# Performance work log

Hardware: AMD Instinct MI355X
Metric: run time of the kernel (lower is better)

## Reference

```python
import jax, jax.numpy as jnp
import numpy as np

D = 1024      # mapped_dim
M = 5         # num_ref_modes
H = 112
W = 112


def setup_inputs() -> dict:
    key = jax.random.key(0)
    ks = jax.random.split(key, 9)
    roi_signal = jax.random.randint(ks[0], (1, 1, H, W), 0, M, dtype=jnp.int32)
    roi_features = jax.random.normal(ks[1], (1, D, H, W), dtype=jnp.float32)
    roi_mask = jax.random.uniform(ks[2], (1, 1, H, W), dtype=jnp.float32)
    s = np.float32(1.0 / np.sqrt(D))
    patch_embed = jax.random.normal(ks[3], (M, D), dtype=jnp.float32) * np.float32(np.sqrt(2.0 / (M + D)))
    Wq = jax.random.normal(ks[4], (D, D), dtype=jnp.float32) * s
    Wk = jax.random.normal(ks[5], (D, D), dtype=jnp.float32) * s
    Wv = jax.random.normal(ks[6], (D, D), dtype=jnp.float32) * s
    bq = jnp.zeros((D,), jnp.float32)
    bk = jnp.zeros((D,), jnp.float32)
    bv = jnp.zeros((D,), jnp.float32)
    conv_w = jax.random.normal(ks[7], (1, D), dtype=jnp.float32) * s  # 1x1 conv, out=1
    conv_b = jnp.zeros((1,), jnp.float32)
    return dict(roi_signal=roi_signal, roi_features=roi_features, roi_mask=roi_mask,
                patch_embed=patch_embed, Wq=Wq, bq=bq, Wk=Wk, bk=bk, Wv=Wv, bv=bv,
                conv_w=conv_w, conv_b=conv_b)


def reference(roi_signal, roi_features, roi_mask, patch_embed, Wq, bq, Wk, bk, Wv, bv, conv_w, conv_b):
    _, _, ROI_H, ROI_W = roi_mask.shape
    d = roi_features.shape[1]
    # ref_embed: one_hot(ref_label) @ patch_embed == gather; (1,1,H,W) -> (1,H,W,D) -> (1,D,H,W)
    pe = jnp.transpose(patch_embed[roi_signal[:, 0]], (0, 3, 1, 2))
    xA = roi_features + pe
    # flatten to tokens: (D, N).T -> (N, D)
    A = xA.reshape(d, -1).T
    O = roi_features.reshape(d, -1).T
    Q = A @ Wq.T + bq
    K = O @ Wk.T + bk
    V = O @ Wv.T + bv
    scores = (Q @ K.T) / jnp.sqrt(jnp.float32(d))        # (N, N) -- dominant intermediate
    attn = jax.nn.softmax(scores, axis=-1)
    out = attn @ V                                        # (N, D)
    # 1x1 conv classification head == per-token dot with conv_w
    seg = (out @ conv_w.T + conv_b).reshape(1, 1, ROI_H, ROI_W)
    return jax.nn.sigmoid(seg.astype(jnp.float32))
```

## Files before the change

### kernel.cpp

```cpp
#include <hip/hip_runtime.h>
#include <math.h>


#define DD 1024
#define NN 12544
#define NSPLIT 5
#define NPART  10
#define NTILES 49

typedef __attribute__((ext_vector_type(8))) short short8;
typedef __attribute__((ext_vector_type(4))) float f32x4;
typedef __attribute__((ext_vector_type(4))) unsigned short ushort4_t;
typedef unsigned short ushort_t;
typedef unsigned int uint32;

__device__ __forceinline__ ushort_t f2bf(float f) {
    union { float f; uint32 u; } v; v.f = f;
    uint32 u = v.u + 0x7FFF + ((v.u >> 16) & 1);
    return (ushort_t)(u >> 16);
}

__device__ __forceinline__ void gload_lds16(const void* g, void* l) {
    __builtin_amdgcn_global_load_lds((const __attribute__((address_space(1))) uint32*)g,
                                     (__attribute__((address_space(3))) uint32*)l, 16, 0, 0);
}

__global__ void k_u(const float* __restrict__ Wv, const float* __restrict__ cw,
                    const float* __restrict__ bv, float* __restrict__ u,
                    float* __restrict__ cptr) {
    const int t = threadIdx.x;
    const int k = blockIdx.x * 256 + t;
    const int d0 = blockIdx.y * 64;
    float acc = 0.f;
#pragma unroll 16
    for (int i = 0; i < 64; ++i) acc += Wv[(size_t)(d0 + i) * DD + k] * cw[d0 + i];
    atomicAdd(&u[k], acc);
    if (blockIdx.x == 0 && t < 64) {
        float ca = bv[d0 + t] * cw[d0 + t];
        for (int off = 32; off > 0; off >>= 1) ca += __shfl_down(ca, off);
        if (t == 0) atomicAdd(cptr, ca);
    }
}

__global__ __launch_bounds__(256)
void k_prep(const float* __restrict__ rf, const int* __restrict__ sig,
            const float* __restrict__ pe, const float* __restrict__ u,
            ushort_t* __restrict__ xo, ushort_t* __restrict__ xa,
            float* __restrict__ vsc) {
    __shared__ ushort_t so[64][136];
    __shared__ ushort_t sa[64][136];
    __shared__ float pel[5 * 128];
    __shared__ float ul[128];
    __shared__ int sigl[64];
    __shared__ f32x4 red[16][16];
    const int t = threadIdx.x;
    const int n0 = blockIdx.x * 64;
    if (t < 64) sigl[t] = sig[n0 + t];
    __syncthreads();
    const int dl = t >> 4, tg = t & 15;
    const int sg[4] = {sigl[tg * 4], sigl[tg * 4 + 1], sigl[tg * 4 + 2], sigl[tg * 4 + 3]};
    const int tok = t >> 2, part = t & 3;
    f32x4 vacc = (f32x4)(0.f);

    for (int c = 0; c < 8; ++c) {
        const int d0 = c * 128;
        for (int i = t; i < 640; i += 256) pel[i] = pe[(i >> 7) * DD + d0 + (i & 127)];
        if (t < 128) ul[t] = u[d0 + t];
        __syncthreads();
#pragma unroll
        for (int s = 0; s < 8; ++s) {
            const int dli = s * 16 + dl;
            const f32x4 x = *(const f32x4*)&rf[(size_t)(d0 + dli) * NN + n0 + tg * 4];
            vacc += x * ul[dli];
            ushort_t oo[4], aa[4];
#pragma unroll
            for (int j = 0; j < 4; ++j) {
                oo[j] = f2bf(x[j]);
                aa[j] = f2bf(x[j] + pel[sg[j] * 128 + dli]);
            }
#pragma unroll
            for (int j = 0; j < 4; ++j) {
                so[tg * 4 + j][dli] = oo[j];
                sa[tg * 4 + j][dli] = aa[j];
            }
        }
        __syncthreads();
#pragma unroll
        for (int i = 0; i < 4; ++i) {
            const int off = part * 32 + i * 8;
            *(short8*)&xo[(size_t)(n0 + tok) * DD + d0 + off] = *(const short8*)&so[tok][off];
            *(short8*)&xa[(size_t)(n0 + tok) * DD + d0 + off] = *(const short8*)&sa[tok][off];
        }
        __syncthreads();
    }
    red[dl][tg] = vacc;
    __syncthreads();
    if (t < 64) {
        float s = 0.f;
#pragma unroll
        for (int i = 0; i < 16; ++i) s += ((const float*)&red[i][t >> 2])[t & 3];
        vsc[n0 + t] = s;
    }
}

__global__ void k_wcast(const float* __restrict__ Wq, const float* __restrict__ Wk,
                        ushort_t* __restrict__ wqb, ushort_t* __restrict__ wkb) {
    const int idx = (blockIdx.x * 256 + threadIdx.x) * 8;
    const float* src = blockIdx.y ? Wk : Wq;
    ushort_t* dst = blockIdx.y ? wkb : wqb;
    f32x4 a = *(const f32x4*)&src[idx];
    f32x4 b = *(const f32x4*)&src[idx + 4];
    short8 o;
#pragma unroll
    for (int j = 0; j < 4; ++j) { o[j] = (short)f2bf(a[j]); o[4 + j] = (short)f2bf(b[j]); }
    *(short8*)&dst[idx] = o;
}

__global__ __launch_bounds__(256, 2)
void k_pgemm(const ushort_t* __restrict__ xb, const ushort_t* __restrict__ wb,
             const float* __restrict__ bias, float scale, ushort_t* __restrict__ outb) {
    __shared__ ushort_t as_[128 * 64];
    __shared__ ushort_t bs_[128 * 64];
    const int t = threadIdx.x;
    const int wv = t >> 6, ln = t & 63;
    const int wr = wv >> 1, wc = wv & 1;
    const int l15 = ln & 15, lhi = ln >> 4;
    const int n0 = blockIdx.x * 128;
    const int m0 = blockIdx.y * 128;
    const int srow = wv * 32;
    const int lr = ln >> 3, lc = ln & 7;
    const int swz = lc ^ lr;

    f32x4 acc[4][4];
#pragma unroll
    for (int a = 0; a < 4; ++a)
#pragma unroll
        for (int b = 0; b < 4; ++b) acc[a][b] = (f32x4)(0.f);

    for (int kk = 0; kk < DD; kk += 64) {
        __syncthreads();
#pragma unroll
        for (int i = 0; i < 4; ++i) {
            const int tok = srow + i * 8 + lr;
            gload_lds16(wb + (size_t)(m0 + tok) * DD + kk + (swz << 3), as_ + (srow + i * 8) * 64);
            gload_lds16(xb + (size_t)(n0 + tok) * DD + kk + (swz << 3), bs_ + (srow + i * 8) * 64);
        }
        __syncthreads();
#pragma unroll
        for (int kp = 0; kp < 2; ++kp) {
            short8 af[4], bf_[4];
#pragma unroll
            for (int mi = 0; mi < 4; ++mi) {
                int r = wr * 64 + mi * 16 + l15;
                int cch = (kp * 4 + lhi) ^ (r & 7);
                af[mi] = *(const short8*)(as_ + r * 64 + cch * 8);
            }
#pragma unroll
            for (int ni = 0; ni < 4; ++ni) {
                int r = wc * 64 + ni * 16 + l15;
                int cch = (kp * 4 + lhi) ^ (r & 7);
                bf_[ni] = *(const short8*)(bs_ + r * 64 + cch * 8);
            }
#pragma unroll
            for (int mi = 0; mi < 4; ++mi)
#pragma unroll
                for (int ni = 0; ni < 4; ++ni)
                    acc[mi][ni] = __builtin_amdgcn_mfma_f32_16x16x32_bf16(
                        af[mi], bf_[ni], acc[mi][ni], 0, 0, 0);
        }
    }
    float bb[4][4];
#pragma unroll
    for (int mi = 0; mi < 4; ++mi) {
        f32x4 b4 = *(const f32x4*)&bias[m0 + wr * 64 + mi * 16 + lhi * 4];
#pragma unroll
        for (int r = 0; r < 4; ++r) bb[mi][r] = b4[r];
    }
#pragma unroll
    for (int mi = 0; mi < 4; ++mi)
#pragma unroll
        for (int ni = 0; ni < 4; ++ni) {
            ushort4_t o;
#pragma unroll
            for (int r = 0; r < 4; ++r) o[r] = f2bf((acc[mi][ni][r] + bb[mi][r]) * scale);
            *(ushort4_t*)&outb[(size_t)(n0 + wc * 64 + ni * 16 + l15) * DD +
                               m0 + wr * 64 + mi * 16 + lhi * 4] = o;
        }
}

__global__ __launch_bounds__(256, 2)
void k_attn(const ushort_t* __restrict__ qb, const ushort_t* __restrict__ kb,
            const float* __restrict__ vsc, float* __restrict__ pl,
            float* __restrict__ pa) {
    __shared__ ushort_t As[3][128 * 32];
    __shared__ ushort_t Bs[3][256 * 32];
    const int t = threadIdx.x;
    const int wv = t >> 6, ln = t & 63;
    const int wm = wv >> 1, wn = wv & 1;
    const int l15 = ln & 15, lhi = ln >> 4;

    const int g = blockIdx.x;
    const int xcd = g & 7, gq = g >> 3;
    const int L = (xcd < 2) ? xcd * 62 + gq : 124 + (xcd - 2) * 61 + gq;
    const int bx = L / NSPLIT, split = L % NSPLIT;
    const int m0 = bx * 128;

    const int srr = ln >> 2;
    const int slc = ln & 3;

    float rl[4][4], ra[4][4];
#pragma unroll
    for (int a = 0; a < 4; ++a)
#pragma unroll
        for (int b = 0; b < 4; ++b) { rl[a][b] = 0.f; ra[a][b] = 0.f; }

    f32x4 acc[4][8];
#pragma unroll
    for (int a = 0; a < 4; ++a)
#pragma unroll
        for (int b = 0; b < 8; ++b) acc[a][b] = (f32x4)(0.f);

#define STAGE(BUF, SNT, KKO)                                                      \
    {                                                                             \
        const int nn0_ = (SNT) * 256;                                             \
        ushort_t* Ad = &As[BUF][0];                                               \
        ushort_t* Bd = &Bs[BUF][0];                                               \
        _Pragma("unroll")                                                         \
        for (int i = 0; i < 2; ++i) {                                             \
            const int row = wv * 32 + i * 16 + srr;                               \
            const int sc = slc ^ ((row >> 1) & 3);                                \
            gload_lds16(qb + (size_t)(m0 + row) * DD + (KKO) + sc * 8,            \
                        Ad + (wv * 32 + i * 16) * 32);                            \
        }                                                                         \
        _Pragma("unroll")                                                         \
        for (int i = 0; i < 4; ++i) {                                             \
            const int row = wv * 64 + i * 16 + srr;                               \
            const int sc = slc ^ ((row >> 1) & 3);                                \
            gload_lds16(kb + (size_t)(nn0_ + row) * DD + (KKO) + sc * 8,          \
                        Bd + (wv * 64 + i * 16) * 32);                            \
        }                                                                         \
    }

    STAGE(0, split, 0);
    STAGE(1, split, 32);
    asm volatile("s_waitcnt vmcnt(6)" ::: "memory");
    __builtin_amdgcn_s_barrier();

    int cur = 0;
    for (int nt = split; nt < NTILES; nt += NSPLIT) {
        const int n0 = nt * 256;
        for (int kidx = 0; kidx < 32; ++kidx) {
            float vv[8];
            if (kidx == 31) {
#pragma unroll
                for (int ni = 0; ni < 8; ++ni) vv[ni] = vsc[n0 + wn * 128 + ni * 16 + l15];
            }
            int nk2 = kidx + 2, nnt2 = nt;
            if (nk2 >= 32) { nk2 -= 32; nnt2 += NSPLIT; }
            const bool st = (nnt2 < NTILES);
            if (st) {
                int b2 = cur + 2; if (b2 >= 3) b2 -= 3;
                STAGE(b2, nnt2, nk2 * 32);
            }
            const ushort_t* Ab = &As[cur][0];
            const ushort_t* Bb = &Bs[cur][0];
            short8 af[4], bfr[8];
#pragma unroll
            for (int mi = 0; mi < 4; ++mi) {
                const int r = wm * 64 + mi * 16 + l15;
                const int c = lhi ^ ((r >> 1) & 3);
                af[mi] = *(const short8*)(Ab + r * 32 + c * 8);
            }
#pragma unroll
            for (int ni = 0; ni < 8; ++ni) {
                const int r = wn * 128 + ni * 16 + l15;
                const int c = lhi ^ ((r >> 1) & 3);
                bfr[ni] = *(const short8*)(Bb + r * 32 + c * 8);
            }
            __builtin_amdgcn_s_setprio(1);
#pragma unroll
            for (int ni = 0; ni < 8; ++ni)
#pragma unroll
                for (int mi = 0; mi < 4; ++mi)
                    acc[mi][ni] = __builtin_amdgcn_mfma_f32_16x16x32_bf16(
                        af[mi], bfr[ni], acc[mi][ni], 0, 0, 0);
            __builtin_amdgcn_s_setprio(0);

            if (kidx == 31) {
#pragma unroll
                for (int mi = 0; mi < 4; ++mi) {
#pragma unroll
                    for (int r = 0; r < 4; ++r) {
                        float sp = 0.f, sv = 0.f;
#pragma unroll
                        for (int ni = 0; ni < 8; ++ni) {
                            float p = __expf(acc[mi][ni][r]);
                            sp += p; sv += p * vv[ni];
                        }
                        sp += __shfl_xor(sp, 1); sv += __shfl_xor(sv, 1);
                        sp += __shfl_xor(sp, 2); sv += __shfl_xor(sv, 2);
                        sp += __shfl_xor(sp, 4); sv += __shfl_xor(sv, 4);
                        sp += __shfl_xor(sp, 8); sv += __shfl_xor(sv, 8);
                        rl[mi][r] += sp;
                        ra[mi][r] += sv;
                    }
                }
#pragma unroll
                for (int a = 0; a < 4; ++a)
#pragma unroll
                    for (int b = 0; b < 8; ++b) acc[a][b] = (f32x4)(0.f);
            }
            if (st) asm volatile("s_waitcnt vmcnt(6)" ::: "memory");
            else    asm volatile("s_waitcnt vmcnt(0)" ::: "memory");
            __builtin_amdgcn_s_barrier();
            cur = (cur + 1 == 3) ? 0 : cur + 1;
        }
    }
#undef STAGE
    if (l15 == 0) {
        const size_t slab = (size_t)(split * 2 + wn) * NN;
#pragma unroll
        for (int mi = 0; mi < 4; ++mi)
#pragma unroll
            for (int r = 0; r < 4; ++r) {
                int row = m0 + wm * 64 + mi * 16 + lhi * 4 + r;
                pl[slab + row] = rl[mi][r];
                pa[slab + row] = ra[mi][r];
            }
    }
}

__global__ void k_comb(const float* __restrict__ pl, const float* __restrict__ pa,
                       const float* __restrict__ cptr, const float* __restrict__ cb,
                       float* __restrict__ out) {
    int n = blockIdx.x * 256 + threadIdx.x;
    float l = 0.f, a = 0.f;
#pragma unroll
    for (int s = 0; s < NPART; ++s) {
        l += pl[(size_t)s * NN + n];
        a += pa[(size_t)s * NN + n];
    }
    float x = a / l + cptr[0] + cb[0];
    out[n] = 1.f / (1.f + __expf(-x));
}

extern "C" void kernel_launch(void* const* d_in, const int* in_sizes, int n_in,
                              void* d_out, int out_size, void* d_ws, size_t ws_size,
                              hipStream_t stream) {
    const int* sig = (const int*)d_in[0];
    const float* rf = (const float*)d_in[1];
    const float* pe = (const float*)d_in[3];
    const float* Wq = (const float*)d_in[4];
    const float* bq = (const float*)d_in[5];
    const float* Wk = (const float*)d_in[6];
    const float* bk = (const float*)d_in[7];
    const float* Wv = (const float*)d_in[8];
    const float* bv = (const float*)d_in[9];
    const float* cw = (const float*)d_in[10];
    const float* cb = (const float*)d_in[11];
    float* out = (float*)d_out;

    ushort_t* buf0 = (ushort_t*)d_ws;
    ushort_t* buf1 = buf0 + (size_t)NN * DD;
    ushort_t* buf2 = buf1 + (size_t)NN * DD;
    ushort_t* wqb = buf2 + (size_t)NN * DD;
    ushort_t* wkb = wqb + (size_t)DD * DD;
    float* u = (float*)(wkb + (size_t)DD * DD);
    float* cptr = u + 1024;
    float* vsc = u + 1024 + 16;
    float* pl = vsc + NN;
    float* pa = pl + (size_t)NPART * NN;

    hipMemsetAsync(u, 0, (1024 + 16) * sizeof(float), stream);
    k_u<<<dim3(4, 16), 256, 0, stream>>>(Wv, cw, bv, u, cptr);
    k_prep<<<196, 256, 0, stream>>>(rf, sig, pe, u, buf0, buf1, vsc);
    k_wcast<<<dim3(512, 2), 256, 0, stream>>>(Wq, Wk, wqb, wkb);
    k_pgemm<<<dim3(98, 8), 256, 0, stream>>>(buf0, wkb, bk, 1.0f, buf2);
    k_pgemm<<<dim3(98, 8), 256, 0, stream>>>(buf1, wqb, bq, 0.03125f, buf0);
    k_attn<<<490, 256, 0, stream>>>(buf0, buf2, vsc, pl, pa);
    k_comb<<<NN / 256, 256, 0, stream>>>(pl, pa, cptr, cb, out);
}
```

Before: 482.6 us.

## Triple-buffer projection GEMM LDS loads with async prefetch two stages ahead

Rewrites the Q/K projection GEMM main loop as a 3-stage software pipeline with K-step 32. Global-to-LDS loads run two stages ahead and use vmcnt waits plus a single barrier per step, instead of two syncthreads around each 64-wide tile. It also raises wave priority around the MFMA block and switches to a new XOR swizzle sized for 32-wide rows. The goal is to hide global load latency behind MFMA work, at the cost of more K iterations and barriers and a hand-managed vmcnt count that must match the number of loads issued.

```diff
diff --git a/kernel.cpp b/kernel.cpp
--- a/kernel.cpp
+++ b/kernel.cpp
@@ -119,17 +119,16 @@
 __global__ __launch_bounds__(256, 2)
 void k_pgemm(const ushort_t* __restrict__ xb, const ushort_t* __restrict__ wb,
              const float* __restrict__ bias, float scale, ushort_t* __restrict__ outb) {
-    __shared__ ushort_t as_[128 * 64];
-    __shared__ ushort_t bs_[128 * 64];
+    __shared__ ushort_t Ws_[3][128 * 32];
+    __shared__ ushort_t Xs_[3][128 * 32];
     const int t = threadIdx.x;
     const int wv = t >> 6, ln = t & 63;
     const int wr = wv >> 1, wc = wv & 1;
     const int l15 = ln & 15, lhi = ln >> 4;
     const int n0 = blockIdx.x * 128;
     const int m0 = blockIdx.y * 128;
-    const int srow = wv * 32;
-    const int lr = ln >> 3, lc = ln & 7;
-    const int swz = lc ^ lr;
+    const int srr = ln >> 2;
+    const int slc = ln & 3;
 
     f32x4 acc[4][4];
 #pragma unroll
@@ -137,38 +136,63 @@
 #pragma unroll
         for (int b = 0; b < 4; ++b) acc[a][b] = (f32x4)(0.f);
 
-    for (int kk = 0; kk < DD; kk += 64) {
-        __syncthreads();
-#pragma unroll
-        for (int i = 0; i < 4; ++i) {
-            const int tok = srow + i * 8 + lr;
-            gload_lds16(wb + (size_t)(m0 + tok) * DD + kk + (swz << 3), as_ + (srow + i * 8) * 64);
-            gload_lds16(xb + (size_t)(n0 + tok) * DD + kk + (swz << 3), bs_ + (srow + i * 8) * 64);
-        }
-        __syncthreads();
-#pragma unroll
-        for (int kp = 0; kp < 2; ++kp) {
-            short8 af[4], bf_[4];
-#pragma unroll
-            for (int mi = 0; mi < 4; ++mi) {
-                int r = wr * 64 + mi * 16 + l15;
-                int cch = (kp * 4 + lhi) ^ (r & 7);
-                af[mi] = *(const short8*)(as_ + r * 64 + cch * 8);
-            }
-#pragma unroll
-            for (int ni = 0; ni < 4; ++ni) {
-                int r = wc * 64 + ni * 16 + l15;
-                int cch = (kp * 4 + lhi) ^ (r & 7);
-                bf_[ni] = *(const short8*)(bs_ + r * 64 + cch * 8);
-            }
-#pragma unroll
-            for (int mi = 0; mi < 4; ++mi)
-#pragma unroll
-                for (int ni = 0; ni < 4; ++ni)
-                    acc[mi][ni] = __builtin_amdgcn_mfma_f32_16x16x32_bf16(
-                        af[mi], bf_[ni], acc[mi][ni], 0, 0, 0);
-        }
-    }
+#define PSTAGE(BUF, KKO)                                                          \
+    {                                                                             \
+        ushort_t* Wd = &Ws_[BUF][0];                                              \
+        ushort_t* Xd = &Xs_[BUF][0];                                              \
+        _Pragma("unroll")                                                         \
+        for (int i = 0; i < 2; ++i) {                                             \
+            const int row = wv * 32 + i * 16 + srr;                               \
+            const int sc = slc ^ ((row >> 1) & 3);                                \
+            gload_lds16(wb + (size_t)(m0 + row) * DD + (KKO) + sc * 8,            \
+                        Wd + (wv * 32 + i * 16) * 32);                            \
+            gload_lds16(xb + (size_t)(n0 + row) * DD + (KKO) + sc * 8,            \
+                        Xd + (wv * 32 + i * 16) * 32);                            \
+        }                                                                         \
+    }
+
+    PSTAGE(0, 0);
+    PSTAGE(1, 32);
+    asm volatile("s_waitcnt vmcnt(4)" ::: "memory");
+    __builtin_amdgcn_s_barrier();
+
+    int cur = 0;
+    for (int kidx = 0; kidx < 32; ++kidx) {
+        const bool st = (kidx + 2 < 32);
+        if (st) {
+            int b2 = cur + 2; if (b2 >= 3) b2 -= 3;
+            PSTAGE(b2, (kidx + 2) * 32);
+        }
+        const ushort_t* Wb = &Ws_[cur][0];
+        const ushort_t* Xb = &Xs_[cur][0];
+        short8 af[4], bf_[4];
+#pragma unroll
+        for (int mi = 0; mi < 4; ++mi) {
+            const int r = wr * 64 + mi * 16 + l15;
+            const int c = lhi ^ ((r >> 1) & 3);
+            af[mi] = *(const short8*)(Wb + r * 32 + c * 8);
+        }
+#pragma unroll
+        for (int ni = 0; ni < 4; ++ni) {
+            const int r = wc * 64 + ni * 16 + l15;
+            const int c = lhi ^ ((r >> 1) & 3);
+            bf_[ni] = *(const short8*)(Xb + r * 32 + c * 8);
+        }
+        __builtin_amdgcn_s_setprio(1);
+#pragma unroll
+        for (int mi = 0; mi < 4; ++mi)
+#pragma unroll
+            for (int ni = 0; ni < 4; ++ni)
+                acc[mi][ni] = __builtin_amdgcn_mfma_f32_16x16x32_bf16(
+                    af[mi], bf_[ni], acc[mi][ni], 0, 0, 0);
+        __builtin_amdgcn_s_setprio(0);
+        if (st) asm volatile("s_waitcnt vmcnt(4)" ::: "memory");
+        else    asm volatile("s_waitcnt vmcnt(0)" ::: "memory");
+        __builtin_amdgcn_s_barrier();
+        cur = (cur + 1 == 3) ? 0 : cur + 1;
+    }
+#undef PSTAGE
+
     float bb[4][4];
 #pragma unroll
     for (int mi = 0; mi < 4; ++mi) {
```

After: 514.7 us. +6.6%, slower.
